# Kernel optimization log

Measured on AMD Instinct MI355X. Metric: run time of the kernel, lower is better.

## Reference

```python
import jax, jax.numpy as jnp
import numpy as np

K = 20  # hard-coded in Codebook.forward


def _renorm(x):
    # x / ||x||_2 along dim 1, matching torch renorm()
    return x / jnp.linalg.norm(x, axis=1, keepdims=True)


def setup_inputs() -> dict:
    key = jax.random.key(0)
    ks = jax.random.split(key, 6)
    B, N, D = 2048, 50000, 128
    z_rot = jax.random.normal(ks[0], (B, D), dtype=jnp.float32)
    z_trans = jax.random.normal(ks[1], (B, D), dtype=jnp.float32)
    # rotation codebook entries are pre-renormed in create_codetensors
    z_rot_book = _renorm(jax.random.normal(ks[2], (N, D), dtype=jnp.float32))
    z_trans_book = jax.random.normal(ks[3], (N, D), dtype=jnp.float32)
    rot_book = jax.random.uniform(ks[4], (N, 1), dtype=jnp.float32) * 360.0
    trans_book = jax.random.normal(ks[5], (N, 3), dtype=jnp.float32)
    return {
        "z_rot": z_rot,
        "z_trans": z_trans,
        "z_rot_book": z_rot_book,
        "z_trans_book": z_trans_book,
        "rot_book": rot_book,
        "trans_book": trans_book,
    }


def reference(z_rot, z_trans, z_rot_book, z_trans_book, rot_book, trans_book):
    # --- get_nearest_cosine ---
    zr = _renorm(z_rot)                                   # [B, D]
    cos = jnp.einsum("bd,nd->bn", zr, z_rot_book)        # [B, N]
    vals_cos, ind_cos = jax.lax.top_k(cos, K)             # [B, K]
    labels_rot = rot_book[ind_cos]                        # [B, K, 1]

    # --- get_nearest_euclidean ---
    # -(||z - b||^2) = -(||z||^2 - 2 z.b + ||b||^2); avoids the [B,N,D]
    # broadcasted intermediate the torch code materializes (same math).
    zq = jnp.sum(z_trans * z_trans, axis=1, keepdims=True)          # [B, 1]
    bq = jnp.sum(z_trans_book * z_trans_book, axis=1)               # [N]
    m2 = 2.0 * jnp.einsum("bd,nd->bn", z_trans, z_trans_book) - zq - bq[None, :]
    vals_euc, ind_euc = jax.lax.top_k(m2, K)              # [B, K]
    labels_trans = trans_book[ind_euc]                    # [B, K, 3]

    return vals_cos, ind_cos, labels_rot, vals_euc, ind_euc, labels_trans
```

## Files before the change

### kernel.cpp

```cpp
#include <hip/hip_runtime.h>
#include <cfloat>
#include <climits>
#include <math.h>

#define BB 2048
#define NN 50000
#define DD 128
#define KK 20

#define NSLICE 16
#define NSL 3125
#define NTILE 98
#define TAILV 21
#define LK 8
#define SLC 16
#define CAND 256
#define K1W 4

#define O_VC 0
#define O_IC 40960
#define O_LR 81920
#define O_VE 122880
#define O_IE 163840
#define O_LT 204800

#define WS_BBF   0
#define WS_BQ2   25690112
#define WS_CAND  25890112

typedef short v8s __attribute__((ext_vector_type(8)));
typedef float v16f __attribute__((ext_vector_type(16)));

union U4V8 { uint4 u; v8s v; };

__device__ __forceinline__ unsigned int bf16rne(float f) {
    unsigned int x = __float_as_uint(f);
    return (x + 0x7FFFu + ((x >> 16) & 1u)) >> 16;
}
__device__ __forceinline__ unsigned int sortkey(float s) {
    unsigned int b = __float_as_uint(s);
    return b ^ ((unsigned int)((int)b >> 31) | 0x80000000u);
}
__device__ __forceinline__ unsigned int med3u(unsigned int a, unsigned int b, unsigned int c) {
    unsigned int d;
    asm("v_med3_u32 %0, %1, %2, %3" : "=v"(d) : "v"(a), "v"(b), "v"(c));
    return d;
}
__device__ __forceinline__ void ins8(unsigned int (&run)[LK], unsigned int k) {
    #pragma unroll
    for (int u = 0; u < LK - 1; u++) run[u] = med3u(k, run[u], run[u + 1]);
    run[LK - 1] = max(k, run[LK - 1]);
}
__device__ __forceinline__ void ce(unsigned int &a, unsigned int &b) {
    unsigned int lo = min(a, b);
    unsigned int hi = max(a, b);
    a = lo; b = hi;
}
__device__ __forceinline__ void merge8(unsigned int (&run)[LK], const unsigned int* s) {
    unsigned int m[8];
    #pragma unroll
    for (int i = 0; i < 8; i++) m[i] = max(run[i], s[7 - i]);
    ce(m[0],m[4]); ce(m[1],m[5]); ce(m[2],m[6]); ce(m[3],m[7]);
    ce(m[0],m[2]); ce(m[1],m[3]); ce(m[4],m[6]); ce(m[5],m[7]);
    ce(m[0],m[1]); ce(m[2],m[3]); ce(m[4],m[5]); ce(m[6],m[7]);
    #pragma unroll
    for (int i = 0; i < 8; i++) run[i] = m[i];
}

__global__ __launch_bounds__(256) void k_cvt2(const float* __restrict__ bR,
                                              const float* __restrict__ bT,
                                              unsigned int* __restrict__ Bbf,
                                              unsigned int* __restrict__ bq2)
{
    const int tile  = blockIdx.x;
    const int slice = blockIdx.y;
    const int task  = blockIdx.z;
    const int t = threadIdx.x;
    const float* __restrict__ src = task ? bT : bR;
    const float sc = task ? 2.f : 1.f;

    __shared__ float ps[4][64];

    unsigned int* tb = Bbf + (((size_t)(task * NSLICE + slice) * NTILE + tile) << 11);

    float partial = 0.f;
    #pragma unroll
    for (int half = 0; half < 2; half++) {
        const int x = t + half * 256;
        const int c = x & 31, hh = (x >> 5) & 1, q = x >> 6;
        const int es = slice * NSL + min(tile * 32 + c, NSL - 1);
        const float* p = src + (size_t)es * DD + q * 16 + hh * 8;
        float4 u0 = *reinterpret_cast<const float4*>(p);
        float4 u1 = *reinterpret_cast<const float4*>(p + 4);
        partial += u0.x * u0.x + u0.y * u0.y + u0.z * u0.z + u0.w * u0.w
                 + u1.x * u1.x + u1.y * u1.y + u1.z * u1.z + u1.w * u1.w;
        uint4 o;
        o.x = bf16rne(u0.x * sc) | (bf16rne(u0.y * sc) << 16);
        o.y = bf16rne(u0.z * sc) | (bf16rne(u0.w * sc) << 16);
        o.z = bf16rne(u1.x * sc) | (bf16rne(u1.y * sc) << 16);
        o.w = bf16rne(u1.z * sc) | (bf16rne(u1.w * sc) << 16);
        *reinterpret_cast<uint4*>(tb + (q << 8) + hh * 128 + c * 4) = o;
    }

    if (task) {
        ps[t >> 6][t & 63] = partial;
        __syncthreads();
        if (t < 32) {
            float sq = 0.f;
            #pragma unroll
            for (int w2 = 0; w2 < 4; w2++) sq += ps[w2][t] + ps[w2][t + 32];
            unsigned int hi = bf16rne(sq);
            float fhi = __uint_as_float(hi << 16);
            unsigned int lo = bf16rne(sq - fhi);
            const int e = slice * NSL + min(tile * 32 + t, NSL - 1);
            bq2[e] = (hi ^ 0x8000u) | ((lo ^ 0x8000u) << 16);
        }
    }
}

__global__ __launch_bounds__(256, 8) void k1_sel(
    const float* __restrict__ zR, const float* __restrict__ zT,
    const unsigned int* __restrict__ Bbf,
    const unsigned int* __restrict__ bq2,
    uint4* __restrict__ candU)
{
    const int slice = blockIdx.x;
    const int rg    = blockIdx.y;
    const int task  = blockIdx.z;
    const int w     = threadIdx.x >> 6;
    const int lane  = threadIdx.x & 63;
    const int col   = lane & 31;
    const int h     = lane >> 5;

    __shared__ uint4 zs[8][64];
    __shared__ unsigned int smk[K1W - 1][64][LK + 1];

    if (w == 0) {
        const float* zp = (task ? zT : zR) + (size_t)(rg * 32 + col) * DD;
        #pragma unroll
        for (int q = 0; q < 8; q++) {
            float4 u0 = *reinterpret_cast<const float4*>(zp + q * 16 + h * 8);
            float4 u1 = *reinterpret_cast<const float4*>(zp + q * 16 + h * 8 + 4);
            uint4 c;
            c.x = bf16rne(u0.x) | (bf16rne(u0.y) << 16);
            c.y = bf16rne(u0.z) | (bf16rne(u0.w) << 16);
            c.z = bf16rne(u1.x) | (bf16rne(u1.y) << 16);
            c.w = bf16rne(u1.z) | (bf16rne(u1.w) << 16);
            zs[q][lane] = c;
        }
    }
    U4V8 zf8; zf8.u = make_uint4(h == 0 ? 0x3F803F80u : 0u, 0u, 0u, 0u);
    __syncthreads();

    unsigned int run[LK];
    #pragma unroll
    for (int u = 0; u < LK; u++) run[u] = 0u;

    const int nbase0 = slice * NSL;
    const unsigned int* bp = Bbf + ((size_t)(task * NSLICE + slice) * NTILE << 11) + lane * 4;

#define TILE_BODY(TILE, TAIL)                                                          \
    {                                                                                  \
        asm volatile("" ::: "memory");   \
        const unsigned int* tb = bp + ((size_t)(TILE) << 11);                          \
        v16f acc = {0.f,0.f,0.f,0.f, 0.f,0.f,0.f,0.f,                                  \
                    0.f,0.f,0.f,0.f, 0.f,0.f,0.f,0.f};                                 \
        _Pragma("unroll")                                                              \
        for (int q = 0; q < 8; q++) {                                                  \
            U4V8 a; a.u = *reinterpret_cast<const uint4*>(tb + (q << 8));              \
            U4V8 z; z.u = zs[q][lane];                                                 \
            acc = __builtin_amdgcn_mfma_f32_32x32x16_bf16(a.v, z.v, acc, 0, 0, 0);     \
        }                                                                              \
        if (task) {                                                                    \
            int e = nbase0 + (TILE) * 32 + col;                                        \
            if (TAIL) e = min(e, nbase0 + NSL - 1);                                    \
            unsigned int bqp = bq2[e];                                                 \
            U4V8 a; a.u = make_uint4(h == 0 ? bqp : 0u, 0u, 0u, 0u);                   \
            acc = __builtin_amdgcn_mfma_f32_32x32x16_bf16(a.v, zf8.v, acc, 0, 0, 0);   \
        }                                                                              \
        const int nb = nbase0 + (TILE) * 32 + 4 * h;                                   \
        _Pragma("unroll")                                                              \
        for (int r = 0; r < 16; r++) {                                                 \
            const int pat = (r & 3) + 8 * (r >> 2);                                    \
            const int n = nb + pat;                                                    \
            unsigned int k = (sortkey(acc[r]) & 0xFFFF0000u) | (unsigned int)n;        \
            if (TAIL && (pat + 4 * h >= TAILV)) k = 0u;                                \
            ins8(run, k);                                                              \
        }                                                                              \
    }

    int tile = w;
    for (; tile < NTILE - 1; tile += K1W) TILE_BODY(tile, 0)
    if (tile == NTILE - 1) TILE_BODY(tile, 1)
#undef TILE_BODY

    if (w > 0) {
        #pragma unroll
        for (int u = 0; u < LK; u++) smk[w - 1][lane][u] = run[u];
    }
    __syncthreads();
    if (w == 0) {
        #pragma unroll
        for (int v = 0; v < K1W - 1; v++) {
            unsigned int s[LK];
            #pragma unroll
            for (int u = 0; u < LK; u++) s[u] = smk[v][lane][u];
            merge8(run, s);
        }

        uint4 o;
        o.x = (run[0] & 0xFFFFu) | ((run[1] & 0xFFFFu) << 16);
        o.y = (run[2] & 0xFFFFu) | ((run[3] & 0xFFFFu) << 16);
        o.z = (run[4] & 0xFFFFu) | ((run[5] & 0xFFFFu) << 16);
        o.w = (run[6] & 0xFFFFu) | ((run[7] & 0xFFFFu) << 16);
        const int row = rg * 32 + col;
        candU[((size_t)(task * BB + row) * NSLICE + slice) * 2 + h] = o;
    }
}

__global__ __launch_bounds__(256) void k2_final(
    const float* __restrict__ Zr, const float* __restrict__ Zt,
    const float* __restrict__ Br, const float* __restrict__ Bt,
    const float* __restrict__ rotB, const float* __restrict__ transB,
    const unsigned short* __restrict__ candU16,
    float* __restrict__ out)
{
    const int row = blockIdx.x;
    const int task = blockIdx.y;
    const int t = threadIdx.x;
    const float* __restrict__ Z  = task ? Zt : Zr;
    const float* __restrict__ Bk = task ? Bt : Br;

    __shared__ __align__(16) float zrow[DD];
    __shared__ int sel[CAND];
    __shared__ double dsum[CAND];
    __shared__ double sval[KK];
    __shared__ int sidx[KK];
    __shared__ float sv[CAND];

    if (t < DD) zrow[t] = Z[(size_t)row * DD + t];
    sel[t] = (int)candU16[((size_t)task * BB + row) * CAND + t];
    __syncthreads();

    if (task == 0) {
        #pragma unroll
        for (int it = 0; it < 8; it++) {
            const int idx = t + it * 256;
            const int cnd = idx >> 3, part = idx & 7;
            const int n = sel[cnd];
            const float* brow = Bk + (size_t)n * DD + part * 16;
            double dp = 0.0;
            #pragma unroll
            for (int q = 0; q < 4; q++) {
                float4 b4 = *reinterpret_cast<const float4*>(brow + q * 4);
                const int k = part * 16 + q * 4;
                dp += (double)zrow[k + 0] * (double)b4.x + (double)zrow[k + 1] * (double)b4.y
                    + (double)zrow[k + 2] * (double)b4.z + (double)zrow[k + 3] * (double)b4.w;
            }
            dp += __shfl_xor(dp, 1, 64);
            dp += __shfl_xor(dp, 2, 64);
            dp += __shfl_xor(dp, 4, 64);
            if ((t & 7) == 0) dsum[cnd] = dp;
        }
        __syncthreads();

        if (t < 64) {
            double zq = (double)zrow[t] * (double)zrow[t]
                      + (double)zrow[t + 64] * (double)zrow[t + 64];
            #pragma unroll
            for (int m = 1; m < 64; m <<= 1) zq += __shfl_xor(zq, m, 64);

            double s[4]; int ix[4];
            #pragma unroll
            for (int j = 0; j < 4; j++) {
                const int c = t + 64 * j;
                s[j] = dsum[c]; ix[j] = sel[c];
            }

            for (int rd = 0; rd < KK; rd++) {
                double bs = s[0]; int bn = ix[0];
                #pragma unroll
                for (int j = 1; j < 4; j++)
                    if (s[j] > bs || (s[j] == bs && ix[j] < bn)) { bs = s[j]; bn = ix[j]; }
                #pragma unroll
                for (int m = 1; m < 64; m <<= 1) {
                    double os = __shfl_xor(bs, m, 64);
                    int on = __shfl_xor(bn, m, 64);
                    if (os > bs || (os == bs && on < bn)) { bs = os; bn = on; }
                }
                #pragma unroll
                for (int j = 0; j < 4; j++) if (ix[j] == bn) s[j] = -DBL_MAX;
                if (t == 0) { sval[rd] = bs; sidx[rd] = bn; }
            }
            if (t == 0) dsum[0] = zq;
        }
        __syncthreads();

        if (t < KK) {
            const double zq = dsum[0];
            const int n = sidx[t];
            const int o = row * KK + t;
            out[O_VC + o] = (float)(sval[t] / sqrt(zq));
            out[O_IC + o] = (float)n;
            out[O_LR + o] = rotB[n];
        }
    } else {
        {
            const int n = sel[t];
            const float* brow = Bk + (size_t)n * DD;
            float L[4], r[8], q[8];
            #pragma unroll
            for (int u = 0; u < 4; u++) L[u] = 0.f;
            #pragma unroll
            for (int u = 0; u < 8; u++) { r[u] = 0.f; q[u] = 0.f; }
            #pragma unroll
            for (int c4 = 0; c4 < 32; c4++) {
                float4 b4 = *reinterpret_cast<const float4*>(brow + c4 * 4);
                float4 z4 = *reinterpret_cast<const float4*>(&zrow[c4 * 4]);
                const int m8 = (c4 & 1) * 4;
                L[0] = __fadd_rn(L[0], __fmul_rn(z4.x, b4.x));
                L[1] = __fadd_rn(L[1], __fmul_rn(z4.y, b4.y));
                L[2] = __fadd_rn(L[2], __fmul_rn(z4.z, b4.z));
                L[3] = __fadd_rn(L[3], __fmul_rn(z4.w, b4.w));
                r[m8 + 0] = __fadd_rn(r[m8 + 0], __fmul_rn(b4.x, b4.x));
                r[m8 + 1] = __fadd_rn(r[m8 + 1], __fmul_rn(b4.y, b4.y));
                r[m8 + 2] = __fadd_rn(r[m8 + 2], __fmul_rn(b4.z, b4.z));
                r[m8 + 3] = __fadd_rn(r[m8 + 3], __fmul_rn(b4.w, b4.w));
                q[m8 + 0] = __fadd_rn(q[m8 + 0], __fmul_rn(z4.x, z4.x));
                q[m8 + 1] = __fadd_rn(q[m8 + 1], __fmul_rn(z4.y, z4.y));
                q[m8 + 2] = __fadd_rn(q[m8 + 2], __fmul_rn(z4.z, z4.z));
                q[m8 + 3] = __fadd_rn(q[m8 + 3], __fmul_rn(z4.w, z4.w));
            }
            const float dot = __fadd_rn(__fadd_rn(L[0], L[2]), __fadd_rn(L[1], L[3]));
            const float bqv = __fadd_rn(__fadd_rn(__fadd_rn(r[0], r[1]), __fadd_rn(r[2], r[3])),
                                        __fadd_rn(__fadd_rn(r[4], r[5]), __fadd_rn(r[6], r[7])));
            const float zqv = __fadd_rn(__fadd_rn(__fadd_rn(q[0], q[1]), __fadd_rn(q[2], q[3])),
                                        __fadd_rn(__fadd_rn(q[4], q[5]), __fadd_rn(q[6], q[7])));
            sv[t] = __fsub_rn(__fsub_rn(__fmul_rn(2.0f, dot), zqv), bqv);
        }
        __syncthreads();

        if (t < 64) {
            float s[4]; int ix[4];
            #pragma unroll
            for (int j = 0; j < 4; j++) { s[j] = sv[t + 64 * j]; ix[j] = sel[t + 64 * j]; }

            for (int rd = 0; rd < KK; rd++) {
                float bs = s[0]; int bn = ix[0];
                #pragma unroll
                for (int j = 1; j < 4; j++)
                    if (s[j] > bs || (s[j] == bs && ix[j] < bn)) { bs = s[j]; bn = ix[j]; }
                #pragma unroll
                for (int m = 1; m < 64; m <<= 1) {
                    float os = __shfl_xor(bs, m, 64);
                    int on = __shfl_xor(bn, m, 64);
                    if (os > bs || (os == bs && on < bn)) { bs = os; bn = on; }
                }
                #pragma unroll
                for (int j = 0; j < 4; j++) if (ix[j] == bn) s[j] = -FLT_MAX;
                if (t == 0) {
                    const int o = row * KK + rd;
                    out[O_VE + o] = bs;
                    out[O_IE + o] = (float)bn;
                    const int o3 = O_LT + o * 3;
                    out[o3 + 0] = transB[bn * 3 + 0];
                    out[o3 + 1] = transB[bn * 3 + 1];
                    out[o3 + 2] = transB[bn * 3 + 2];
                }
            }
        }
    }
}

extern "C" void kernel_launch(void* const* d_in, const int* in_sizes, int n_in,
                              void* d_out, int out_size, void* d_ws, size_t ws_size,
                              hipStream_t stream) {
    const float* zR = (const float*)d_in[0];
    const float* zT = (const float*)d_in[1];
    const float* bR = (const float*)d_in[2];
    const float* bT = (const float*)d_in[3];
    const float* rotB = (const float*)d_in[4];
    const float* transB = (const float*)d_in[5];
    float* out = (float*)d_out;

    char* ws = (char*)d_ws;
    unsigned int* Bbf = (unsigned int*)(ws + WS_BBF);
    unsigned int* bq2 = (unsigned int*)(ws + WS_BQ2);
    uint4* candU = (uint4*)(ws + WS_CAND);

    k_cvt2<<<dim3(NTILE, NSLICE, 2), 256, 0, stream>>>(bR, bT, Bbf, bq2);
    k1_sel<<<dim3(NSLICE, 64, 2), 256, 0, stream>>>(zR, zT, Bbf, bq2, candU);
    k2_final<<<dim3(BB, 2), 256, 0, stream>>>(zR, zT, bR, bT, rotB, transB,
                                              (const unsigned short*)candU, out);
}
```

Before: 343.8 us.

## Stage candidate codebook rows through padded LDS in the rerank kernel

The rerank kernel now loads the 256 candidate codebook rows in four chunks of 64. Four threads copy each row into a padded shared-memory buffer with float4 loads, which makes the global reads more contiguous. The rotation and translation dot products then read from LDS. The translation path is split across four lanes per row and reduced with shuffles, which changes the parallel layout while keeping the same float summation grouping. This adds about 33 KB of LDS and extra barriers, which may reduce occupancy.

```diff
diff --git a/kernel.cpp b/kernel.cpp
--- a/kernel.cpp
+++ b/kernel.cpp
@@ -27,6 +27,8 @@
 #define WS_BBF   0
 #define WS_BQ2   25690112
 #define WS_CAND  25890112
+
+#define BSTR 132
 
 typedef short v8s __attribute__((ext_vector_type(8)));
 typedef float v16f __attribute__((ext_vector_type(16)));
@@ -237,33 +239,83 @@
     __shared__ double sval[KK];
     __shared__ int sidx[KK];
     __shared__ float sv[CAND];
+    __shared__ __align__(16) float buf[64 * BSTR];
 
     if (t < DD) zrow[t] = Z[(size_t)row * DD + t];
     sel[t] = (int)candU16[((size_t)task * BB + row) * CAND + t];
     __syncthreads();
 
+    const int sr = t >> 2;
+    const int sg = t & 3;
+
+    for (int c = 0; c < 4; ++c) {
+        {
+            const int n = sel[c * 64 + sr];
+            const float* src = Bk + (size_t)n * DD + sg * 32;
+            float4 tmp[8];
+            #pragma unroll
+            for (int i = 0; i < 8; i++)
+                tmp[i] = *reinterpret_cast<const float4*>(src + i * 4);
+            #pragma unroll
+            for (int i = 0; i < 8; i++)
+                *reinterpret_cast<float4*>(&buf[sr * BSTR + sg * 32 + i * 4]) = tmp[i];
+        }
+        __syncthreads();
+
+        if (task == 0) {
+            #pragma unroll
+            for (int sub = 0; sub < 2; sub++) {
+                const int idx = c * 512 + sub * 256 + t;
+                const int cnd = idx >> 3, part = idx & 7;
+                const float* brow = &buf[(cnd - c * 64) * BSTR + part * 16];
+                double dp = 0.0;
+                #pragma unroll
+                for (int q = 0; q < 4; q++) {
+                    float4 b4 = *reinterpret_cast<const float4*>(brow + q * 4);
+                    const int k = part * 16 + q * 4;
+                    dp += (double)zrow[k + 0] * (double)b4.x + (double)zrow[k + 1] * (double)b4.y
+                        + (double)zrow[k + 2] * (double)b4.z + (double)zrow[k + 3] * (double)b4.w;
+                }
+                dp += __shfl_xor(dp, 1, 64);
+                dp += __shfl_xor(dp, 2, 64);
+                dp += __shfl_xor(dp, 4, 64);
+                if ((t & 7) == 0) dsum[cnd] = dp;
+            }
+        } else {
+            const float* brow = &buf[sr * BSTR];
+            float L = 0.f, rA = 0.f, rB = 0.f, qA = 0.f, qB = 0.f;
+            #pragma unroll
+            for (int c4 = 0; c4 < 32; c4++) {
+                const float b = brow[c4 * 4 + sg];
+                const float z = zrow[c4 * 4 + sg];
+                L = __fadd_rn(L, __fmul_rn(z, b));
+                if ((c4 & 1) == 0) {
+                    rA = __fadd_rn(rA, __fmul_rn(b, b));
+                    qA = __fadd_rn(qA, __fmul_rn(z, z));
+                } else {
+                    rB = __fadd_rn(rB, __fmul_rn(b, b));
+                    qB = __fadd_rn(qB, __fmul_rn(z, z));
+                }
+            }
+            float a2 = __fadd_rn(L, __shfl_xor(L, 2, 64));
+            float dot = __fadd_rn(a2, __shfl_xor(a2, 1, 64));
+            float s1 = __fadd_rn(rA, __shfl_xor(rA, 1, 64));
+            float u1 = __fadd_rn(s1, __shfl_xor(s1, 2, 64));
+            float s2 = __fadd_rn(rB, __shfl_xor(rB, 1, 64));
+            float u2 = __fadd_rn(s2, __shfl_xor(s2, 2, 64));
+            const float bqv = __fadd_rn(u1, u2);
+            float s3 = __fadd_rn(qA, __shfl_xor(qA, 1, 64));
+            float u3 = __fadd_rn(s3, __shfl_xor(s3, 2, 64));
+            float s4 = __fadd_rn(qB, __shfl_xor(qB, 1, 64));
+            float u4 = __fadd_rn(s4, __shfl_xor(s4, 2, 64));
+            const float zqv = __fadd_rn(u3, u4);
+            if (sg == 0)
+                sv[c * 64 + sr] = __fsub_rn(__fsub_rn(__fmul_rn(2.0f, dot), zqv), bqv);
+        }
+        __syncthreads();
+    }
+
     if (task == 0) {
-        #pragma unroll
-        for (int it = 0; it < 8; it++) {
-            const int idx = t + it * 256;
-            const int cnd = idx >> 3, part = idx & 7;
-            const int n = sel[cnd];
-            const float* brow = Bk + (size_t)n * DD + part * 16;
-            double dp = 0.0;
-            #pragma unroll
-            for (int q = 0; q < 4; q++) {
-                float4 b4 = *reinterpret_cast<const float4*>(brow + q * 4);
-                const int k = part * 16 + q * 4;
-                dp += (double)zrow[k + 0] * (double)b4.x + (double)zrow[k + 1] * (double)b4.y
-                    + (double)zrow[k + 2] * (double)b4.z + (double)zrow[k + 3] * (double)b4.w;
-            }
-            dp += __shfl_xor(dp, 1, 64);
-            dp += __shfl_xor(dp, 2, 64);
-            dp += __shfl_xor(dp, 4, 64);
-            if ((t & 7) == 0) dsum[cnd] = dp;
-        }
-        __syncthreads();
-
         if (t < 64) {
             double zq = (double)zrow[t] * (double)zrow[t]
                       + (double)zrow[t + 64] * (double)zrow[t + 64];
@@ -273,8 +325,8 @@
             double s[4]; int ix[4];
             #pragma unroll
             for (int j = 0; j < 4; j++) {
-                const int c = t + 64 * j;
-                s[j] = dsum[c]; ix[j] = sel[c];
+                const int cc = t + 64 * j;
+                s[j] = dsum[cc]; ix[j] = sel[cc];
             }
 
             for (int rd = 0; rd < KK; rd++) {
@@ -305,41 +357,6 @@
             out[O_LR + o] = rotB[n];
         }
     } else {
-        {
-            const int n = sel[t];
-            const float* brow = Bk + (size_t)n * DD;
-            float L[4], r[8], q[8];
-            #pragma unroll
-            for (int u = 0; u < 4; u++) L[u] = 0.f;
-            #pragma unroll
-            for (int u = 0; u < 8; u++) { r[u] = 0.f; q[u] = 0.f; }
-            #pragma unroll
-            for (int c4 = 0; c4 < 32; c4++) {
-                float4 b4 = *reinterpret_cast<const float4*>(brow + c4 * 4);
-                float4 z4 = *reinterpret_cast<const float4*>(&zrow[c4 * 4]);
-                const int m8 = (c4 & 1) * 4;
-                L[0] = __fadd_rn(L[0], __fmul_rn(z4.x, b4.x));
-                L[1] = __fadd_rn(L[1], __fmul_rn(z4.y, b4.y));
-                L[2] = __fadd_rn(L[2], __fmul_rn(z4.z, b4.z));
-                L[3] = __fadd_rn(L[3], __fmul_rn(z4.w, b4.w));
-                r[m8 + 0] = __fadd_rn(r[m8 + 0], __fmul_rn(b4.x, b4.x));
-                r[m8 + 1] = __fadd_rn(r[m8 + 1], __fmul_rn(b4.y, b4.y));
-                r[m8 + 2] = __fadd_rn(r[m8 + 2], __fmul_rn(b4.z, b4.z));
-                r[m8 + 3] = __fadd_rn(r[m8 + 3], __fmul_rn(b4.w, b4.w));
-                q[m8 + 0] = __fadd_rn(q[m8 + 0], __fmul_rn(z4.x, z4.x));
-                q[m8 + 1] = __fadd_rn(q[m8 + 1], __fmul_rn(z4.y, z4.y));
-                q[m8 + 2] = __fadd_rn(q[m8 + 2], __fmul_rn(z4.z, z4.z));
-                q[m8 + 3] = __fadd_rn(q[m8 + 3], __fmul_rn(z4.w, z4.w));
-            }
-            const float dot = __fadd_rn(__fadd_rn(L[0], L[2]), __fadd_rn(L[1], L[3]));
-            const float bqv = __fadd_rn(__fadd_rn(__fadd_rn(r[0], r[1]), __fadd_rn(r[2], r[3])),
-                                        __fadd_rn(__fadd_rn(r[4], r[5]), __fadd_rn(r[6], r[7])));
-            const float zqv = __fadd_rn(__fadd_rn(__fadd_rn(q[0], q[1]), __fadd_rn(q[2], q[3])),
-                                        __fadd_rn(__fadd_rn(q[4], q[5]), __fadd_rn(q[6], q[7])));
-            sv[t] = __fsub_rn(__fsub_rn(__fmul_rn(2.0f, dot), zqv), bqv);
-        }
-        __syncthreads();
-
         if (t < 64) {
             float s[4]; int ix[4];
             #pragma unroll
```

New measurement: 335.4 us. 2.4% less time.

## Prune rescoring candidates with key-based threshold and batch sorted-merge selection

Applied to the files above, without the earlier changes.

The selection kernel now gathers each tile's 16 scores, sorts them in two 8-wide networks and merges them into the running top-8, replacing per-element med3 insertion. It writes the top four full keys plus 12-bit packed indices for the remaining candidates. The final kernel uses the stored bf16 score keys to estimate the 20th-best score and a conservative error bound, and only rescores candidates above that threshold in full precision. Each candidate's dot product is now done by one thread instead of eight cooperating threads. This cuts codebook gathers and FP64 work, but relies on hand-tuned error margins whose correctness depends on the input distribution.

```diff
diff --git a/kernel.cpp b/kernel.cpp
--- a/kernel.cpp
+++ b/kernel.cpp
@@ -13,7 +13,6 @@
 #define NTILE 98
 #define TAILV 21
 #define LK 8
-#define SLC 16
 #define CAND 256
 #define K1W 4
 
@@ -26,7 +25,8 @@
 
 #define WS_BBF   0
 #define WS_BQ2   25690112
-#define WS_CAND  25890112
+#define WS_CANDT 25890112
+#define WS_CANDB 27987264
 
 typedef short v8s __attribute__((ext_vector_type(8)));
 typedef float v16f __attribute__((ext_vector_type(16)));
@@ -41,20 +41,22 @@
     unsigned int b = __float_as_uint(s);
     return b ^ ((unsigned int)((int)b >> 31) | 0x80000000u);
 }
-__device__ __forceinline__ unsigned int med3u(unsigned int a, unsigned int b, unsigned int c) {
-    unsigned int d;
-    asm("v_med3_u32 %0, %1, %2, %3" : "=v"(d) : "v"(a), "v"(b), "v"(c));
-    return d;
-}
-__device__ __forceinline__ void ins8(unsigned int (&run)[LK], unsigned int k) {
-    #pragma unroll
-    for (int u = 0; u < LK - 1; u++) run[u] = med3u(k, run[u], run[u + 1]);
-    run[LK - 1] = max(k, run[LK - 1]);
+__device__ __forceinline__ float unkey(unsigned int k) {
+    unsigned int b = (k & 0x80000000u) ? (k ^ 0x80000000u) : ~k;
+    return __uint_as_float(b);
 }
 __device__ __forceinline__ void ce(unsigned int &a, unsigned int &b) {
     unsigned int lo = min(a, b);
     unsigned int hi = max(a, b);
     a = lo; b = hi;
+}
+__device__ __forceinline__ void sort8(unsigned int* k) {
+    ce(k[0],k[1]); ce(k[2],k[3]); ce(k[4],k[5]); ce(k[6],k[7]);
+    ce(k[0],k[2]); ce(k[1],k[3]); ce(k[4],k[6]); ce(k[5],k[7]);
+    ce(k[1],k[2]); ce(k[5],k[6]);
+    ce(k[0],k[4]); ce(k[1],k[5]); ce(k[2],k[6]); ce(k[3],k[7]);
+    ce(k[2],k[4]); ce(k[3],k[5]);
+    ce(k[1],k[2]); ce(k[3],k[4]); ce(k[5],k[6]);
 }
 __device__ __forceinline__ void merge8(unsigned int (&run)[LK], const unsigned int* s) {
     unsigned int m[8];
@@ -122,7 +124,7 @@
     const float* __restrict__ zR, const float* __restrict__ zT,
     const unsigned int* __restrict__ Bbf,
     const unsigned int* __restrict__ bq2,
-    uint4* __restrict__ candU)
+    uint4* __restrict__ candT, unsigned short* __restrict__ candB)
 {
     const int slice = blockIdx.x;
     const int rg    = blockIdx.y;
@@ -179,14 +181,17 @@
             acc = __builtin_amdgcn_mfma_f32_32x32x16_bf16(a.v, zf8.v, acc, 0, 0, 0);   \
         }                                                                              \
         const int nb = nbase0 + (TILE) * 32 + 4 * h;                                   \
+        unsigned int kk[16];                                                           \
         _Pragma("unroll")                                                              \
         for (int r = 0; r < 16; r++) {                                                 \
             const int pat = (r & 3) + 8 * (r >> 2);                                    \
             const int n = nb + pat;                                                    \
             unsigned int k = (sortkey(acc[r]) & 0xFFFF0000u) | (unsigned int)n;        \
             if (TAIL && (pat + 4 * h >= TAILV)) k = 0u;                                \
-            ins8(run, k);                                                              \
+            kk[r] = k;                                                                 \
         }                                                                              \
+        sort8(&kk[0]); sort8(&kk[8]);                                                  \
+        merge8(run, &kk[0]); merge8(run, &kk[8]);                                      \
     }
 
     int tile = w;
@@ -208,13 +213,17 @@
             merge8(run, s);
         }
 
-        uint4 o;
-        o.x = (run[0] & 0xFFFFu) | ((run[1] & 0xFFFFu) << 16);
-        o.y = (run[2] & 0xFFFFu) | ((run[3] & 0xFFFFu) << 16);
-        o.z = (run[4] & 0xFFFFu) | ((run[5] & 0xFFFFu) << 16);
-        o.w = (run[6] & 0xFFFFu) | ((run[7] & 0xFFFFu) << 16);
         const int row = rg * 32 + col;
-        candU[((size_t)(task * BB + row) * NSLICE + slice) * 2 + h] = o;
+        const size_t strm = (((size_t)(task * BB + row) * NSLICE + slice) << 1) + h;
+        candT[strm] = make_uint4(run[7], run[6], run[5], run[4]);
+        unsigned long long V =
+              (unsigned long long)((run[3] & 0xFFFFu) - (unsigned)nbase0)
+            | ((unsigned long long)((run[2] & 0xFFFFu) - (unsigned)nbase0) << 12)
+            | ((unsigned long long)((run[1] & 0xFFFFu) - (unsigned)nbase0) << 24)
+            | ((unsigned long long)((run[0] & 0xFFFFu) - (unsigned)nbase0) << 36);
+        candB[strm * 3 + 0] = (unsigned short)V;
+        candB[strm * 3 + 1] = (unsigned short)(V >> 16);
+        candB[strm * 3 + 2] = (unsigned short)(V >> 32);
     }
 }
 
@@ -222,7 +231,8 @@
     const float* __restrict__ Zr, const float* __restrict__ Zt,
     const float* __restrict__ Br, const float* __restrict__ Bt,
     const float* __restrict__ rotB, const float* __restrict__ transB,
-    const unsigned short* __restrict__ candU16,
+    const unsigned int* __restrict__ candT32,
+    const unsigned short* __restrict__ candB,
     float* __restrict__ out)
 {
     const int row = blockIdx.x;
@@ -232,51 +242,128 @@
     const float* __restrict__ Bk = task ? Bt : Br;
 
     __shared__ __align__(16) float zrow[DD];
-    __shared__ int sel[CAND];
-    __shared__ double dsum[CAND];
+    __shared__ unsigned int keyT[128];
+    __shared__ double dsc[CAND];
+    __shared__ float svc[CAND];
+    __shared__ int sidn[CAND];
     __shared__ double sval[KK];
     __shared__ int sidx[KK];
-    __shared__ float sv[CAND];
+    __shared__ float thr;
+    __shared__ double zqs;
 
     if (t < DD) zrow[t] = Z[(size_t)row * DD + t];
-    sel[t] = (int)candU16[((size_t)task * BB + row) * CAND + t];
-    __syncthreads();
-
-    if (task == 0) {
+    if (t < 128) keyT[t] = candT32[(size_t)(task * BB + row) * 128 + t];
+    __syncthreads();
+
+    if (t < 64) {
+        double zq = (double)zrow[t] * (double)zrow[t]
+                  + (double)zrow[t + 64] * (double)zrow[t + 64];
         #pragma unroll
-        for (int it = 0; it < 8; it++) {
-            const int idx = t + it * 256;
-            const int cnd = idx >> 3, part = idx & 7;
-            const int n = sel[cnd];
-            const float* brow = Bk + (size_t)n * DD + part * 16;
-            double dp = 0.0;
+        for (int m = 1; m < 64; m <<= 1) zq += __shfl_xor(zq, m, 64);
+
+        unsigned int a = keyT[t], b = keyT[t + 64];
+        unsigned int t20 = 0u;
+        for (int rd = 0; rd < KK; rd++) {
+            unsigned int mx = max(a, b);
             #pragma unroll
-            for (int q = 0; q < 4; q++) {
-                float4 b4 = *reinterpret_cast<const float4*>(brow + q * 4);
-                const int k = part * 16 + q * 4;
-                dp += (double)zrow[k + 0] * (double)b4.x + (double)zrow[k + 1] * (double)b4.y
-                    + (double)zrow[k + 2] * (double)b4.z + (double)zrow[k + 3] * (double)b4.w;
-            }
-            dp += __shfl_xor(dp, 1, 64);
-            dp += __shfl_xor(dp, 2, 64);
-            dp += __shfl_xor(dp, 4, 64);
-            if ((t & 7) == 0) dsum[cnd] = dp;
-        }
-        __syncthreads();
-
-        if (t < 64) {
-            double zq = (double)zrow[t] * (double)zrow[t]
-                      + (double)zrow[t + 64] * (double)zrow[t + 64];
-            #pragma unroll
-            for (int m = 1; m < 64; m <<= 1) zq += __shfl_xor(zq, m, 64);
-
+            for (int m = 1; m < 64; m <<= 1)
+                mx = max(mx, (unsigned int)__shfl_xor((int)mx, m, 64));
+            if (a == mx) a = 0u;
+            if (b == mx) b = 0u;
+            t20 = mx;
+        }
+        if (t == 0) {
+            zqs = zq;
+            const float s20 = unkey(t20 & 0xFFFF0000u);
+            const float nz = sqrtf((float)zq);
+            const float Bm = task ? (0.14f * nz + 0.05f) : (0.0045f * nz + 0.001f);
+            thr = s20 - 2.f * Bm - 0.016f * fabsf(s20) - (task ? 0.1f : 1e-3f);
+        }
+    }
+    __syncthreads();
+
+    {
+        const int c = t, s = c >> 3, r = c & 7, slice = s >> 1;
+        const float thv = thr;
+        bool keep;
+        int idx;
+        if (r < 4) {
+            const unsigned int k = keyT[s * 4 + r];
+            idx = (int)(k & 0xFFFFu);
+            keep = unkey(k & 0xFFFF0000u) >= thv;
+        } else {
+            const unsigned short* cb = candB + ((size_t)(task * BB + row) * 32 + s) * 3;
+            unsigned long long V = (unsigned long long)cb[0]
+                | ((unsigned long long)cb[1] << 16)
+                | ((unsigned long long)cb[2] << 32);
+            idx = slice * NSL + (int)((V >> (12 * (r - 4))) & 0xFFFu);
+            keep = unkey(keyT[s * 4 + 3] & 0xFFFF0000u) >= thv;
+        }
+        sidn[c] = idx;
+
+        if (task == 0) {
+            double dp = -DBL_MAX;
+            if (keep) {
+                const float* brow = Bk + (size_t)idx * DD;
+                dp = 0.0;
+                #pragma unroll
+                for (int q = 0; q < 32; q++) {
+                    float4 b4 = *reinterpret_cast<const float4*>(brow + q * 4);
+                    float4 z4 = *reinterpret_cast<const float4*>(&zrow[q * 4]);
+                    dp += (double)z4.x * (double)b4.x + (double)z4.y * (double)b4.y
+                        + (double)z4.z * (double)b4.z + (double)z4.w * (double)b4.w;
+                }
+            }
+            dsc[c] = dp;
+        } else {
+            float v = -FLT_MAX;
+            if (keep) {
+                const float* brow = Bk + (size_t)idx * DD;
+                float L[4], rr[8], qq[8];
+                #pragma unroll
+                for (int u = 0; u < 4; u++) L[u] = 0.f;
+                #pragma unroll
+                for (int u = 0; u < 8; u++) { rr[u] = 0.f; qq[u] = 0.f; }
+                #pragma unroll
+                for (int c4 = 0; c4 < 32; c4++) {
+                    float4 b4 = *reinterpret_cast<const float4*>(brow + c4 * 4);
+                    float4 z4 = *reinterpret_cast<const float4*>(&zrow[c4 * 4]);
+                    const int m8 = (c4 & 1) * 4;
+                    L[0] = __fadd_rn(L[0], __fmul_rn(z4.x, b4.x));
+                    L[1] = __fadd_rn(L[1], __fmul_rn(z4.y, b4.y));
+                    L[2] = __fadd_rn(L[2], __fmul_rn(z4.z, b4.z));
+                    L[3] = __fadd_rn(L[3], __fmul_rn(z4.w, b4.w));
+                    rr[m8 + 0] = __fadd_rn(rr[m8 + 0], __fmul_rn(b4.x, b4.x));
+                    rr[m8 + 1] = __fadd_rn(rr[m8 + 1], __fmul_rn(b4.y, b4.y));
+                    rr[m8 + 2] = __fadd_rn(rr[m8 + 2], __fmul_rn(b4.z, b4.z));
+                    rr[m8 + 3] = __fadd_rn(rr[m8 + 3], __fmul_rn(b4.w, b4.w));
+                    qq[m8 + 0] = __fadd_rn(qq[m8 + 0], __fmul_rn(z4.x, z4.x));
+                    qq[m8 + 1] = __fadd_rn(qq[m8 + 1], __fmul_rn(z4.y, z4.y));
+                    qq[m8 + 2] = __fadd_rn(qq[m8 + 2], __fmul_rn(z4.z, z4.z));
+                    qq[m8 + 3] = __fadd_rn(qq[m8 + 3], __fmul_rn(z4.w, z4.w));
+                }
+                const float dot = __fadd_rn(__fadd_rn(L[0], L[2]), __fadd_rn(L[1], L[3]));
+                const float bqv = __fadd_rn(
+                    __fadd_rn(__fadd_rn(rr[0], rr[1]), __fadd_rn(rr[2], rr[3])),
+                    __fadd_rn(__fadd_rn(rr[4], rr[5]), __fadd_rn(rr[6], rr[7])));
+                const float zqv = __fadd_rn(
+                    __fadd_rn(__fadd_rn(qq[0], qq[1]), __fadd_rn(qq[2], qq[3])),
+                    __fadd_rn(__fadd_rn(qq[4], qq[5]), __fadd_rn(qq[6], qq[7])));
+                v = __fsub_rn(__fsub_rn(__fmul_rn(2.0f, dot), zqv), bqv);
+            }
+            svc[c] = v;
+        }
+    }
+    __syncthreads();
+
+    if (t < 64) {
+        if (task == 0) {
             double s[4]; int ix[4];
             #pragma unroll
             for (int j = 0; j < 4; j++) {
-                const int c = t + 64 * j;
-                s[j] = dsum[c]; ix[j] = sel[c];
-            }
-
+                const int cc = t + 64 * j;
+                s[j] = dsc[cc]; ix[j] = sidn[cc];
+            }
             for (int rd = 0; rd < KK; rd++) {
                 double bs = s[0]; int bn = ix[0];
                 #pragma unroll
@@ -292,59 +379,13 @@
                 for (int j = 0; j < 4; j++) if (ix[j] == bn) s[j] = -DBL_MAX;
                 if (t == 0) { sval[rd] = bs; sidx[rd] = bn; }
             }
-            if (t == 0) dsum[0] = zq;
-        }
-        __syncthreads();
-
-        if (t < KK) {
-            const double zq = dsum[0];
-            const int n = sidx[t];
-            const int o = row * KK + t;
-            out[O_VC + o] = (float)(sval[t] / sqrt(zq));
-            out[O_IC + o] = (float)n;
-            out[O_LR + o] = rotB[n];
-        }
-    } else {
-        {
-            const int n = sel[t];
-            const float* brow = Bk + (size_t)n * DD;
-            float L[4], r[8], q[8];
-            #pragma unroll
-            for (int u = 0; u < 4; u++) L[u] = 0.f;
-            #pragma unroll
-            for (int u = 0; u < 8; u++) { r[u] = 0.f; q[u] = 0.f; }
-            #pragma unroll
-            for (int c4 = 0; c4 < 32; c4++) {
-                float4 b4 = *reinterpret_cast<const float4*>(brow + c4 * 4);
-                float4 z4 = *reinterpret_cast<const float4*>(&zrow[c4 * 4]);
-                const int m8 = (c4 & 1) * 4;
-                L[0] = __fadd_rn(L[0], __fmul_rn(z4.x, b4.x));
-                L[1] = __fadd_rn(L[1], __fmul_rn(z4.y, b4.y));
-                L[2] = __fadd_rn(L[2], __fmul_rn(z4.z, b4.z));
-                L[3] = __fadd_rn(L[3], __fmul_rn(z4.w, b4.w));
-                r[m8 + 0] = __fadd_rn(r[m8 + 0], __fmul_rn(b4.x, b4.x));
-                r[m8 + 1] = __fadd_rn(r[m8 + 1], __fmul_rn(b4.y, b4.y));
-                r[m8 + 2] = __fadd_rn(r[m8 + 2], __fmul_rn(b4.z, b4.z));
-                r[m8 + 3] = __fadd_rn(r[m8 + 3], __fmul_rn(b4.w, b4.w));
-                q[m8 + 0] = __fadd_rn(q[m8 + 0], __fmul_rn(z4.x, z4.x));
-                q[m8 + 1] = __fadd_rn(q[m8 + 1], __fmul_rn(z4.y, z4.y));
-                q[m8 + 2] = __fadd_rn(q[m8 + 2], __fmul_rn(z4.z, z4.z));
-                q[m8 + 3] = __fadd_rn(q[m8 + 3], __fmul_rn(z4.w, z4.w));
-            }
-            const float dot = __fadd_rn(__fadd_rn(L[0], L[2]), __fadd_rn(L[1], L[3]));
-            const float bqv = __fadd_rn(__fadd_rn(__fadd_rn(r[0], r[1]), __fadd_rn(r[2], r[3])),
-                                        __fadd_rn(__fadd_rn(r[4], r[5]), __fadd_rn(r[6], r[7])));
-            const float zqv = __fadd_rn(__fadd_rn(__fadd_rn(q[0], q[1]), __fadd_rn(q[2], q[3])),
-                                        __fadd_rn(__fadd_rn(q[4], q[5]), __fadd_rn(q[6], q[7])));
-            sv[t] = __fsub_rn(__fsub_rn(__fmul_rn(2.0f, dot), zqv), bqv);
-        }
-        __syncthreads();
-
-        if (t < 64) {
+        } else {
             float s[4]; int ix[4];
             #pragma unroll
-            for (int j = 0; j < 4; j++) { s[j] = sv[t + 64 * j]; ix[j] = sel[t + 64 * j]; }
-
+            for (int j = 0; j < 4; j++) {
+                const int cc = t + 64 * j;
+                s[j] = svc[cc]; ix[j] = sidn[cc];
+            }
             for (int rd = 0; rd < KK; rd++) {
                 float bs = s[0]; int bn = ix[0];
                 #pragma unroll
@@ -370,6 +411,15 @@
             }
         }
     }
+    __syncthreads();
+
+    if (task == 0 && t < KK) {
+        const int n = sidx[t];
+        const int o = row * KK + t;
+        out[O_VC + o] = (float)(sval[t] / sqrt(zqs));
+        out[O_IC + o] = (float)n;
+        out[O_LR + o] = rotB[n];
+    }
 }
 
 extern "C" void kernel_launch(void* const* d_in, const int* in_sizes, int n_in,
@@ -386,10 +436,11 @@
     char* ws = (char*)d_ws;
     unsigned int* Bbf = (unsigned int*)(ws + WS_BBF);
     unsigned int* bq2 = (unsigned int*)(ws + WS_BQ2);
-    uint4* candU = (uint4*)(ws + WS_CAND);
+    uint4* candT = (uint4*)(ws + WS_CANDT);
+    unsigned short* candB = (unsigned short*)(ws + WS_CANDB);
 
     k_cvt2<<<dim3(NTILE, NSLICE, 2), 256, 0, stream>>>(bR, bT, Bbf, bq2);
-    k1_sel<<<dim3(NSLICE, 64, 2), 256, 0, stream>>>(zR, zT, Bbf, bq2, candU);
+    k1_sel<<<dim3(NSLICE, 64, 2), 256, 0, stream>>>(zR, zT, Bbf, bq2, candT, candB);
     k2_final<<<dim3(BB, 2), 256, 0, stream>>>(zR, zT, bR, bT, rotB, transB,
-                                              (const unsigned short*)candU, out);
-}
+                                              (const unsigned int*)candT, candB, out);
+}
```

Result: slower. 385.0 us (+12.0%).
